# Kernel tuning notes

Hardware: AMD Instinct MI355X
Metric: run time of the kernel (lower is better)

The kernel has to match this reference:

```python
import jax, jax.numpy as jnp
import numpy as np

H, N, CH, RANK = 512, 64, 1, 1
SEQ_L = 4096


def setup_inputs() -> dict:
    key = jax.random.key(0)
    k0, k1, k2, k3, k4 = jax.random.split(key, 5)
    # A = -exp(A_real) + i*A_imag  (real_transform='exp'); HiPPO-style imag init
    A_real = jnp.log(0.5 + jax.random.uniform(k0, (H, N), dtype=jnp.float32))
    A_imag = jnp.broadcast_to(np.pi * jnp.arange(N, dtype=jnp.float32), (H, N)).copy()
    # complex params stored as (..., 2) real/imag pairs (torch.view_as_real layout)
    B = (0.5 ** 0.5) * jax.random.normal(k1, (1, H, N, 2), dtype=jnp.float32)
    C = jax.random.normal(k2, (CH, H, N, 2), dtype=jnp.float32)
    P = (0.5 ** 0.5) * jax.random.normal(k3, (RANK, H, N, 2), dtype=jnp.float32)
    # dt = exp(inv_dt) log-uniform in [1e-3, 1e-1]  (dt_transform='exp')
    lo, hi = np.log(1e-3), np.log(1e-1)
    inv_dt = (lo + (hi - lo) * jax.random.uniform(k4, (H,), dtype=jnp.float32)).astype(jnp.float32)
    return {"A_real": A_real, "A_imag": A_imag, "B": B, "C": C, "P": P,
            "inv_dt": inv_dt, "L": SEQ_L}


def _c(x):
    # view_as_complex
    return x[..., 0] + 1j * x[..., 1]


def _s4_kernel(A_real, A_imag, B, C, P, inv_dt, L):
    dt = jnp.exp(inv_dt)                       # (H,)
    A = -jnp.exp(A_real) + 1j * A_imag          # (H, N) complex64
    Bc, Cc, Pc = _c(B), _c(C), _c(P)            # (1,H,N), (CH,H,N), (R,H,N)
    Q = jnp.conj(Pc)

    Lf = L // 2 + 1
    omega = jnp.exp(-2j * jnp.pi / L) ** jnp.arange(Lf)   # FFT nodes, (Lf,)
    z = 2 * (1 - omega) / (1 + omega)                      # bilinear-transform freqs

    A_dt = A * dt[:, None]                     # (H, N)
    Bcat = jnp.concatenate([Bc, Pc], axis=0)   # (1+R, H, N)
    Ccat = jnp.concatenate([Cc, Q], axis=0)    # (CH+R, H, N)
    v = Bcat[:, None] * Ccat[None]             # (1+R, CH+R, H, N)
    v = v * dt[:, None]

    # Cauchy kernel with implicit conjugate-pair symmetry:
    #   r[a,b,h,l] = sum_n v/(z - A_dt) + conj(v)/(z - conj(A_dt))
    denom = 1.0 / (z - A_dt[..., None])                    # (H, N, Lf)
    r = jnp.einsum('abhn,hnl->abhl', v, denom)
    denom_c = 1.0 / (z - jnp.conj(A_dt)[..., None])
    r = r + jnp.einsum('abhn,hnl->abhl', jnp.conj(v), denom_c)

    # rank-1 Woodbury correction
    k_f = r[:-1, :-1] - r[:-1, -1:] * r[-1:, :-1] / (1 + r[-1:, -1:])
    k_f = k_f * 2 / (1 + omega)

    k = jnp.fft.irfft(k_f, n=L)                # (1, CH, H, L) real
    k = k[..., :L]
    return k[-1]                               # k_B: (CH, H, L)


def reference(A_real, A_imag, B, C, P, inv_dt, L):
    return _s4_kernel(A_real, A_imag, B, C, P, inv_dt, L)
```

## Files before the change

kernel.cpp:

```cpp
#include <hip/hip_runtime.h>
#include <math.h>

namespace {
constexpr int kH = 512;
constexpr int kN = 64;
constexpr int kL = 4096;
constexpr int kM = 2048;
constexpr int kPairRec = 40;
constexpr int kThreads = 256;
constexpr int kFftThreads = 512;
constexpr float kPi = 3.14159265358979323846f;
}

typedef float v2f __attribute__((ext_vector_type(2)));

__device__ __forceinline__ int lpad(int i) { return i + (i >> 4); }
__device__ __forceinline__ v2f fma2(v2f a, v2f b, v2f c) {
    return __builtin_elementwise_fma(a, b, c);
}

__global__ __launch_bounds__(64)
void s4_prep(const float* __restrict__ A_real, const float* __restrict__ A_imag,
             const float* __restrict__ Bv, const float* __restrict__ Cv,
             const float* __restrict__ Pv, const float* __restrict__ inv_dt,
             float* __restrict__ cst)
{
    const int h = blockIdx.x;
    const int n = threadIdx.x;
    const int idx = h * kN + n;
    const float dt = expf(inv_dt[h]);
    const float ar = -expf(A_real[idx]) * dt;
    const float ai =  A_imag[idx] * dt;
    const float br = Bv[idx*2+0], bi = Bv[idx*2+1];
    const float cr = Cv[idx*2+0], ci = Cv[idx*2+1];
    const float pr = Pv[idx*2+0], pi = Pv[idx*2+1];
    const float v00r = (br*cr - bi*ci)*dt, v00i = (br*ci + bi*cr)*dt;
    const float v01r = (br*pr + bi*pi)*dt, v01i = (bi*pr - br*pi)*dt;
    const float v10r = (pr*cr - pi*ci)*dt, v10i = (pr*ci + pi*cr)*dt;
    const float v11r = (pr*pr + pi*pi)*dt;
    const float ar2 = ar*ar;
    const float C1  = ar2 + ai*ai;
    const float dd  = ar2 - ai*ai;

    float co[16];
    co[0]  = -2.f*C1*(v00r*ar + v00i*ai);   co[1]  = 2.f*(v00i*ai - v00r*ar);
    co[2]  = -4.f*v00r*dd - 8.f*v00i*ar*ai; co[3]  = -4.f*v00r;
    co[4]  = -2.f*C1*(v01r*ar + v01i*ai);   co[5]  = 2.f*(v01i*ai - v01r*ar);
    co[6]  = -4.f*v01r*dd - 8.f*v01i*ar*ai; co[7]  = -4.f*v01r;
    co[8]  = -2.f*C1*(v10r*ar + v10i*ai);   co[9]  = 2.f*(v10i*ai - v10r*ar);
    co[10] = -4.f*v10r*dd - 8.f*v10i*ar*ai; co[11] = -4.f*v10r;
    co[12] = -2.f*C1*(v11r*ar);             co[13] = -2.f*v11r*ar;
    co[14] = -4.f*v11r*dd;                  co[15] = -4.f*v11r;

    float* base = cst + ((size_t)h * (kN/2) + (n >> 1)) * kPairRec + (n & 1);
    base[0] = ai;
    base[2] = ar2;
    #pragma unroll
    for (int k = 0; k < 16; ++k) base[4 + 2*k] = co[k];
}

__global__ __launch_bounds__(kThreads)
void s4_spectrum(const float* __restrict__ cst, float2* __restrict__ Xg)
{
    const int h   = blockIdx.x >> 2;
    const int q   = blockIdx.x & 3;
    const int tid = threadIdx.x;
    const int la  = q * 512 + tid;

    float tv[2], sv[2];
    v2f t2p[2];
    #pragma unroll
    for (int b = 0; b < 2; ++b) {
        const int l = la + 256 * b;
        float sn, cn;
        sincosf((float)l * (kPi / (float)kL), &sn, &cn);
        tv[b] = sn / cn;
        const float t2 = 2.f * tv[b];
        sv[b] = t2 * t2;
        t2p[b] = (v2f){t2, t2};
    }

    v2f A0[2][4], A1[2][4], B0[2][4], B1[2][4];
    #pragma unroll
    for (int b = 0; b < 2; ++b)
        #pragma unroll
        for (int p = 0; p < 4; ++p) {
            A0[b][p] = (v2f){0.f, 0.f}; A1[b][p] = (v2f){0.f, 0.f};
            B0[b][p] = (v2f){0.f, 0.f}; B1[b][p] = (v2f){0.f, 0.f};
        }

    const v2f* rec = (const v2f*)(cst + (size_t)h * (kN/2) * kPairRec);
    #pragma unroll 2
    for (int j = 0; j < kN/2; ++j) {
        const v2f* r = rec + j * (kPairRec/2);
        const v2f aip  = r[0];
        const v2f ar2p = r[1];
        #pragma unroll
        for (int b = 0; b < 2; ++b) {
            const v2f w1 = t2p[b] - aip;
            const v2f w2 = t2p[b] + aip;
            const v2f m1 = fma2(w1, w1, ar2p);
            const v2f m2 = fma2(w2, w2, ar2p);
            const v2f D  = m1 * m2;
            v2f qv;
            qv.x = __builtin_amdgcn_rcpf(D.x);
            qv.y = __builtin_amdgcn_rcpf(D.y);
            #pragma unroll
            for (int p = 0; p < 4; ++p) {
                A0[b][p] = fma2(r[2 + 4*p + 0], qv, A0[b][p]);
                A1[b][p] = fma2(r[2 + 4*p + 1], qv, A1[b][p]);
                B0[b][p] = fma2(r[2 + 4*p + 2], qv, B0[b][p]);
                B1[b][p] = fma2(r[2 + 4*p + 3], qv, B1[b][p]);
            }
        }
    }

    #pragma unroll
    for (int b = 0; b < 2; ++b) {
        const int l = la + 256 * b;
        const float t = tv[b];
        const v2f sp = (v2f){sv[b], sv[b]};
        const v2f r00 = fma2(sp, A1[b][0], A0[b][0]);
        const v2f i00 = fma2(sp, B1[b][0], B0[b][0]);
        const v2f r01 = fma2(sp, A1[b][1], A0[b][1]);
        const v2f i01 = fma2(sp, B1[b][1], B0[b][1]);
        const v2f r10 = fma2(sp, A1[b][2], A0[b][2]);
        const v2f i10 = fma2(sp, B1[b][2], B0[b][2]);
        const v2f r11 = fma2(sp, A1[b][3], A0[b][3]);
        const v2f i11 = fma2(sp, B1[b][3], B0[b][3]);
        const float s00r = r00.x + r00.y, s00i = t * (i00.x + i00.y);
        const float s01r = r01.x + r01.y, s01i = t * (i01.x + i01.y);
        const float s10r = r10.x + r10.y, s10i = t * (i10.x + i10.y);
        const float s11r = r11.x + r11.y, s11i = t * (i11.x + i11.y);
        const float nr = s01r*s10r - s01i*s10i;
        const float ni = s01r*s10i + s01i*s10r;
        const float dr = 1.f + s11r, di = s11i;
        const float qd = __builtin_amdgcn_rcpf(fmaf(dr, dr, di*di));
        const float wr = (nr*dr + ni*di) * qd;
        const float wi = (ni*dr - nr*di) * qd;
        const float gr = s00r - wr, gi = s00i - wi;
        Xg[h*kM + l] = make_float2(fmaf(-gi, t, gr), fmaf(gr, t, gi));
    }
}

__global__ __launch_bounds__(kFftThreads)
void s4_ifft(const float* __restrict__ Bv,
             const float* __restrict__ Cv,
             const float* __restrict__ inv_dt,
             float* __restrict__ out)
{
    __shared__ float2 W2[kM + kM / 16];
    __shared__ float2 TW[kM / 2 + kM / 32];
    __shared__ float  XnyqR;

    const int h   = blockIdx.x;
    const int tid = threadIdx.x;
    const float2* Xg = (const float2*)(out + (size_t)h * kL);

    if (tid < kN) {
        const int idx = h * kN + tid;
        const float dt = expf(inv_dt[h]);
        const float br = Bv[idx*2+0], bi = Bv[idx*2+1];
        const float cr = Cv[idx*2+0], ci = Cv[idx*2+1];
        float vr = (br*cr - bi*ci) * dt;
        #pragma unroll
        for (int off = 32; off > 0; off >>= 1) vr += __shfl_down(vr, off, 64);
        if (tid == 0) XnyqR = vr;
    }
    for (int j = tid; j < kM / 2; j += kFftThreads) {
        float s, c;
        sincosf((2.0f * kPi / (float)kM) * (float)j, &s, &c);
        TW[lpad(j)] = make_float2(c, s);
    }
    __syncthreads();

    for (int k = tid; k <= kM / 2; k += kFftThreads) {
        const float2 Xa = Xg[k];
        const float2 Xb = (k == 0) ? make_float2(XnyqR, 0.0f) : Xg[kM - k];
        const float Er = 0.5f * (Xa.x + Xb.x);
        const float Ei = 0.5f * (Xa.y - Xb.y);
        const float Dr = 0.5f * (Xa.x - Xb.x);
        const float Di = 0.5f * (Xa.y + Xb.y);
        float s, c;
        sincosf((2.0f * kPi / (float)kL) * (float)k, &s, &c);
        const float Or = c * Dr - s * Di;
        const float Oi = c * Di + s * Dr;
        const int rk = (int)(__brev((unsigned)k) >> 21);
        W2[lpad(rk)] = make_float2(Er - Oi, Ei + Or);
        if (k != 0 && k != kM / 2) {
            const int rmk = (int)(__brev((unsigned)(kM - k)) >> 21);
            W2[lpad(rmk)] = make_float2(Er + Oi, Or - Ei);
        }
    }
    __syncthreads();

    for (int hs = 1; hs < kM; hs <<= 1) {
        const int tw_stride = (kM / 2) / hs;
        for (int j = tid; j < kM / 2; j += kFftThreads) {
            const int pos = j & (hs - 1);
            const int grp = j / hs;
            const int i0  = grp * 2 * hs + pos;
            const int i1  = i0 + hs;
            const float2 tw = TW[lpad(pos * tw_stride)];
            const float2 a = W2[lpad(i0)];
            const float2 b = W2[lpad(i1)];
            const float tr = tw.x * b.x - tw.y * b.y;
            const float ti = tw.x * b.y + tw.y * b.x;
            W2[lpad(i0)] = make_float2(a.x + tr, a.y + ti);
            W2[lpad(i1)] = make_float2(a.x - tr, a.y - ti);
        }
        __syncthreads();
    }

    const float invM = 1.0f / (float)kM;
    float2* out2 = (float2*)(out + (size_t)h * kL);
    for (int n = tid; n < kM; n += kFftThreads) {
        const float2 zn = W2[lpad(n)];
        out2[n] = make_float2(zn.x * invM, zn.y * invM);
    }
}

extern "C" void kernel_launch(void* const* d_in, const int* in_sizes, int n_in,
                              void* d_out, int out_size, void* d_ws, size_t ws_size,
                              hipStream_t stream) {
    const float* A_real = (const float*)d_in[0];
    const float* A_imag = (const float*)d_in[1];
    const float* B      = (const float*)d_in[2];
    const float* C      = (const float*)d_in[3];
    const float* P      = (const float*)d_in[4];
    const float* inv_dt = (const float*)d_in[5];
    float* out = (float*)d_out;

    float* cst = (float*)d_ws;

    s4_prep<<<dim3(kH), dim3(64), 0, stream>>>(A_real, A_imag, B, C, P, inv_dt,
                                               cst);
    s4_spectrum<<<dim3(kH * 4), dim3(kThreads), 0, stream>>>(cst, (float2*)out);
    s4_ifft<<<dim3(kH), dim3(kFftThreads), 0, stream>>>(B, C, inv_dt, out);
}
```

Before: 113.4 us.

## Use one frequency per thread in spectrum kernel and radix-4 iFFT stages

The spectrum kernel now gives each thread a single frequency and launches twice as many blocks, where before each thread handled two frequencies. This adds parallelism and lowers register pressure, but coefficient loads are no longer shared across two frequencies. The in-block inverse FFT replaces eleven radix-2 passes with five radix-4 passes plus one final radix-2 pass, which cuts barriers and shared-memory round trips. The radix-4 twiddle is built by squaring the stored twiddle, which may slightly change rounding.

```diff
diff --git a/kernel.cpp b/kernel.cpp
--- a/kernel.cpp
+++ b/kernel.cpp
@@ -17,6 +17,9 @@
 __device__ __forceinline__ int lpad(int i) { return i + (i >> 4); }
 __device__ __forceinline__ v2f fma2(v2f a, v2f b, v2f c) {
     return __builtin_elementwise_fma(a, b, c);
+}
+__device__ __forceinline__ float2 cmul(float2 a, float2 b) {
+    return make_float2(a.x*b.x - a.y*b.y, a.x*b.y + a.y*b.x);
 }
 
 __global__ __launch_bounds__(64)
@@ -62,32 +65,24 @@
 __global__ __launch_bounds__(kThreads)
 void s4_spectrum(const float* __restrict__ cst, float2* __restrict__ Xg)
 {
-    const int h   = blockIdx.x >> 2;
-    const int q   = blockIdx.x & 3;
+    const int h   = blockIdx.x >> 3;
+    const int q   = blockIdx.x & 7;
     const int tid = threadIdx.x;
-    const int la  = q * 512 + tid;
-
-    float tv[2], sv[2];
-    v2f t2p[2];
+    const int l   = q * 256 + tid;
+
+    float sn, cn;
+    sincosf((float)l * (kPi / (float)kL), &sn, &cn);
+    const float t  = sn / cn;
+    const float t2 = 2.f * t;
+    const float s  = t2 * t2;
+    const v2f t2p  = (v2f){t2, t2};
+
+    v2f A0[4], A1[4], B0[4], B1[4];
     #pragma unroll
-    for (int b = 0; b < 2; ++b) {
-        const int l = la + 256 * b;
-        float sn, cn;
-        sincosf((float)l * (kPi / (float)kL), &sn, &cn);
-        tv[b] = sn / cn;
-        const float t2 = 2.f * tv[b];
-        sv[b] = t2 * t2;
-        t2p[b] = (v2f){t2, t2};
-    }
-
-    v2f A0[2][4], A1[2][4], B0[2][4], B1[2][4];
-    #pragma unroll
-    for (int b = 0; b < 2; ++b)
-        #pragma unroll
-        for (int p = 0; p < 4; ++p) {
-            A0[b][p] = (v2f){0.f, 0.f}; A1[b][p] = (v2f){0.f, 0.f};
-            B0[b][p] = (v2f){0.f, 0.f}; B1[b][p] = (v2f){0.f, 0.f};
-        }
+    for (int p = 0; p < 4; ++p) {
+        A0[p] = (v2f){0.f, 0.f}; A1[p] = (v2f){0.f, 0.f};
+        B0[p] = (v2f){0.f, 0.f}; B1[p] = (v2f){0.f, 0.f};
+    }
 
     const v2f* rec = (const v2f*)(cst + (size_t)h * (kN/2) * kPairRec);
     #pragma unroll 2
@@ -95,52 +90,44 @@
         const v2f* r = rec + j * (kPairRec/2);
         const v2f aip  = r[0];
         const v2f ar2p = r[1];
+        const v2f w1 = t2p - aip;
+        const v2f w2 = t2p + aip;
+        const v2f m1 = fma2(w1, w1, ar2p);
+        const v2f m2 = fma2(w2, w2, ar2p);
+        const v2f D  = m1 * m2;
+        v2f qv;
+        qv.x = __builtin_amdgcn_rcpf(D.x);
+        qv.y = __builtin_amdgcn_rcpf(D.y);
         #pragma unroll
-        for (int b = 0; b < 2; ++b) {
-            const v2f w1 = t2p[b] - aip;
-            const v2f w2 = t2p[b] + aip;
-            const v2f m1 = fma2(w1, w1, ar2p);
-            const v2f m2 = fma2(w2, w2, ar2p);
-            const v2f D  = m1 * m2;
-            v2f qv;
-            qv.x = __builtin_amdgcn_rcpf(D.x);
-            qv.y = __builtin_amdgcn_rcpf(D.y);
-            #pragma unroll
-            for (int p = 0; p < 4; ++p) {
-                A0[b][p] = fma2(r[2 + 4*p + 0], qv, A0[b][p]);
-                A1[b][p] = fma2(r[2 + 4*p + 1], qv, A1[b][p]);
-                B0[b][p] = fma2(r[2 + 4*p + 2], qv, B0[b][p]);
-                B1[b][p] = fma2(r[2 + 4*p + 3], qv, B1[b][p]);
-            }
+        for (int p = 0; p < 4; ++p) {
+            A0[p] = fma2(r[2 + 4*p + 0], qv, A0[p]);
+            A1[p] = fma2(r[2 + 4*p + 1], qv, A1[p]);
+            B0[p] = fma2(r[2 + 4*p + 2], qv, B0[p]);
+            B1[p] = fma2(r[2 + 4*p + 3], qv, B1[p]);
         }
     }
 
-    #pragma unroll
-    for (int b = 0; b < 2; ++b) {
-        const int l = la + 256 * b;
-        const float t = tv[b];
-        const v2f sp = (v2f){sv[b], sv[b]};
-        const v2f r00 = fma2(sp, A1[b][0], A0[b][0]);
-        const v2f i00 = fma2(sp, B1[b][0], B0[b][0]);
-        const v2f r01 = fma2(sp, A1[b][1], A0[b][1]);
-        const v2f i01 = fma2(sp, B1[b][1], B0[b][1]);
-        const v2f r10 = fma2(sp, A1[b][2], A0[b][2]);
-        const v2f i10 = fma2(sp, B1[b][2], B0[b][2]);
-        const v2f r11 = fma2(sp, A1[b][3], A0[b][3]);
-        const v2f i11 = fma2(sp, B1[b][3], B0[b][3]);
-        const float s00r = r00.x + r00.y, s00i = t * (i00.x + i00.y);
-        const float s01r = r01.x + r01.y, s01i = t * (i01.x + i01.y);
-        const float s10r = r10.x + r10.y, s10i = t * (i10.x + i10.y);
-        const float s11r = r11.x + r11.y, s11i = t * (i11.x + i11.y);
-        const float nr = s01r*s10r - s01i*s10i;
-        const float ni = s01r*s10i + s01i*s10r;
-        const float dr = 1.f + s11r, di = s11i;
-        const float qd = __builtin_amdgcn_rcpf(fmaf(dr, dr, di*di));
-        const float wr = (nr*dr + ni*di) * qd;
-        const float wi = (ni*dr - nr*di) * qd;
-        const float gr = s00r - wr, gi = s00i - wi;
-        Xg[h*kM + l] = make_float2(fmaf(-gi, t, gr), fmaf(gr, t, gi));
-    }
+    const v2f sp = (v2f){s, s};
+    const v2f r00 = fma2(sp, A1[0], A0[0]);
+    const v2f i00 = fma2(sp, B1[0], B0[0]);
+    const v2f r01 = fma2(sp, A1[1], A0[1]);
+    const v2f i01 = fma2(sp, B1[1], B0[1]);
+    const v2f r10 = fma2(sp, A1[2], A0[2]);
+    const v2f i10 = fma2(sp, B1[2], B0[2]);
+    const v2f r11 = fma2(sp, A1[3], A0[3]);
+    const v2f i11 = fma2(sp, B1[3], B0[3]);
+    const float s00r = r00.x + r00.y, s00i = t * (i00.x + i00.y);
+    const float s01r = r01.x + r01.y, s01i = t * (i01.x + i01.y);
+    const float s10r = r10.x + r10.y, s10i = t * (i10.x + i10.y);
+    const float s11r = r11.x + r11.y, s11i = t * (i11.x + i11.y);
+    const float nr = s01r*s10r - s01i*s10i;
+    const float ni = s01r*s10i + s01i*s10r;
+    const float dr = 1.f + s11r, di = s11i;
+    const float qd = __builtin_amdgcn_rcpf(fmaf(dr, dr, di*di));
+    const float wr = (nr*dr + ni*di) * qd;
+    const float wi = (ni*dr - nr*di) * qd;
+    const float gr = s00r - wr, gi = s00i - wi;
+    Xg[h*kM + l] = make_float2(fmaf(-gi, t, gr), fmaf(gr, t, gi));
 }
 
 __global__ __launch_bounds__(kFftThreads)
@@ -194,23 +181,44 @@
     }
     __syncthreads();
 
-    for (int hs = 1; hs < kM; hs <<= 1) {
-        const int tw_stride = (kM / 2) / hs;
-        for (int j = tid; j < kM / 2; j += kFftThreads) {
+    #pragma unroll
+    for (int lg = 0; lg <= 8; lg += 2) {
+        const int hs = 1 << lg;
+        const int twstride = 512 >> lg;
+        for (int j = tid; j < kM / 4; j += kFftThreads) {
             const int pos = j & (hs - 1);
-            const int grp = j / hs;
-            const int i0  = grp * 2 * hs + pos;
-            const int i1  = i0 + hs;
-            const float2 tw = TW[lpad(pos * tw_stride)];
-            const float2 a = W2[lpad(i0)];
-            const float2 b = W2[lpad(i1)];
-            const float tr = tw.x * b.x - tw.y * b.y;
-            const float ti = tw.x * b.y + tw.y * b.x;
-            W2[lpad(i0)] = make_float2(a.x + tr, a.y + ti);
-            W2[lpad(i1)] = make_float2(a.x - tr, a.y - ti);
+            const int grp = j >> lg;
+            const int i0  = grp * 4 * hs + pos;
+            const float2 e0 = W2[lpad(i0)];
+            const float2 e1 = W2[lpad(i0 + hs)];
+            const float2 e2 = W2[lpad(i0 + 2*hs)];
+            const float2 e3 = W2[lpad(i0 + 3*hs)];
+            const float2 wB = TW[lpad(pos * twstride)];
+            const float2 wA = cmul(wB, wB);
+            const float2 t1 = cmul(wA, e1);
+            const float2 t3 = cmul(wA, e3);
+            const float2 a0 = make_float2(e0.x + t1.x, e0.y + t1.y);
+            const float2 a1 = make_float2(e0.x - t1.x, e0.y - t1.y);
+            const float2 a2 = make_float2(e2.x + t3.x, e2.y + t3.y);
+            const float2 a3 = make_float2(e2.x - t3.x, e2.y - t3.y);
+            const float2 u2 = cmul(wB, a2);
+            const float2 u3 = cmul(wB, a3);
+            W2[lpad(i0)]        = make_float2(a0.x + u2.x, a0.y + u2.y);
+            W2[lpad(i0 + 2*hs)] = make_float2(a0.x - u2.x, a0.y - u2.y);
+            W2[lpad(i0 + hs)]   = make_float2(a1.x - u3.y, a1.y + u3.x);
+            W2[lpad(i0 + 3*hs)] = make_float2(a1.x + u3.y, a1.y - u3.x);
         }
         __syncthreads();
     }
+    for (int j = tid; j < kM / 2; j += kFftThreads) {
+        const float2 tw = TW[lpad(j)];
+        const float2 a  = W2[lpad(j)];
+        const float2 b  = W2[lpad(j + 1024)];
+        const float2 tb = cmul(tw, b);
+        W2[lpad(j)]        = make_float2(a.x + tb.x, a.y + tb.y);
+        W2[lpad(j + 1024)] = make_float2(a.x - tb.x, a.y - tb.y);
+    }
+    __syncthreads();
 
     const float invM = 1.0f / (float)kM;
     float2* out2 = (float2*)(out + (size_t)h * kL);
@@ -235,6 +243,6 @@
 
     s4_prep<<<dim3(kH), dim3(64), 0, stream>>>(A_real, A_imag, B, C, P, inv_dt,
                                                cst);
-    s4_spectrum<<<dim3(kH * 4), dim3(kThreads), 0, stream>>>(cst, (float2*)out);
+    s4_spectrum<<<dim3(kH * 8), dim3(kThreads), 0, stream>>>(cst, (float2*)out);
     s4_ifft<<<dim3(kH), dim3(kFftThreads), 0, stream>>>(B, C, inv_dt, out);
 }
```

New measurement: 115.8 us. 2.1% more time.
